# Kernel optimization log

Measured on AMD Instinct MI355X. Metric: run time of the kernel, lower is better.

## Reference

```python
import jax, jax.numpy as jnp
import numpy as np

B, S = 1, 2048
HID, INTER = 4096, 11008
HEADS, HD = 32, 128
GS = 128
EPS = 1e-6
BASE = 10000.0
IMIN, IMAX = -(2**31), 2**31 - 1


def _rope_tables():
    inv_freq = 1.0 / (BASE ** (np.arange(0, HD, 2, dtype=np.float32) / HD))
    t = np.arange(S, dtype=np.float32)
    freqs = np.outer(t, inv_freq)            # [S, HD/2]
    emb = np.concatenate([freqs, freqs], -1)  # [S, HD]
    return jnp.asarray(np.sin(emb), jnp.float32), jnp.asarray(np.cos(emb), jnp.float32)


def setup_inputs() -> dict:
    key = jax.random.key(0)
    ks = iter(jax.random.split(key, 40))
    def qset(in_f, out_f):
        qw = jax.random.randint(next(ks), (in_f // 8, out_f), IMIN, IMAX, dtype=jnp.int32)
        qz = jax.random.randint(next(ks), (in_f // GS, out_f // 8), IMIN, IMAX, dtype=jnp.int32)
        sc = jax.random.uniform(next(ks), (in_f // GS, out_f), dtype=jnp.float32) * 0.01 + 1e-3
        return qw, qz, sc
    dims = {"q": (HID, HID), "k": (HID, HID), "v": (HID, HID), "o": (HID, HID),
            "gate": (HID, INTER), "up": (HID, INTER), "down": (INTER, HID)}
    inp = {}
    for name, (i, o) in dims.items():
        qw, qz, sc = qset(i, o)
        inp["qw_" + name] = qw
        inp["qz_" + name] = qz
        inp["sc_" + name] = sc
    inp["hidden_states"] = jax.random.normal(next(ks), (B, S, HID), dtype=jnp.float32)
    inp["ln1_w"] = jnp.ones((HID,), jnp.float32)
    inp["ln2_w"] = jnp.ones((HID,), jnp.float32)
    sin, cos = _rope_tables()
    inp["sin"] = sin
    inp["cos"] = cos
    # causal additive mask, as stored in ExLlamaBuffer.attn_mask (past_len = 0)
    mask = jnp.where(jnp.tril(jnp.ones((S, S), bool)), 0.0, -1e9).astype(jnp.float32)
    inp["attn_mask"] = mask[None, None]
    return inp


def _dequant(qw, qz, sc):
    # GPTQ int4: qweight [in/8, out] packs 8 rows per int32; qzeros [groups, out/8]
    in_f, out_f = qw.shape[0] * 8, qw.shape[1]
    groups = sc.shape[0]
    sh = jnp.arange(8, dtype=jnp.int32) * 4
    w = ((qw[:, None, :] >> sh[None, :, None]) & 15)
    w = w.reshape(groups, in_f // groups, out_f).astype(jnp.float32)
    z = ((qz[:, :, None] >> sh[None, None, :]) & 15).reshape(groups, out_f).astype(jnp.float32)
    return ((w - (z + 1.0)[:, None, :]) * sc[:, None, :]).reshape(in_f, out_f)


def _rms(x, w):
    v = jnp.mean(x * x, axis=-1, keepdims=True)
    return x * jax.lax.rsqrt(v + EPS) * w


def _rot_half(x):
    x1, x2 = jnp.split(x, 2, axis=-1)
    return jnp.concatenate([-x2, x1], axis=-1)


def reference(qw_q, qz_q, sc_q, qw_k, qz_k, sc_k, qw_v, qz_v, sc_v,
              qw_o, qz_o, sc_o, qw_gate, qz_gate, sc_gate,
              qw_up, qz_up, sc_up, qw_down, qz_down, sc_down,
              hidden_states, ln1_w, ln2_w, sin, cos, attn_mask):
    lin = lambda x, a, b, c: x @ _dequant(a, b, c)
    h = hidden_states
    # attention block
    x = _rms(h, ln1_w)
    q = lin(x, qw_q, qz_q, sc_q).reshape(B, S, HEADS, HD).transpose(0, 2, 1, 3)
    k = lin(x, qw_k, qz_k, sc_k).reshape(B, S, HEADS, HD).transpose(0, 2, 1, 3)
    v = lin(x, qw_v, qz_v, sc_v).reshape(B, S, HEADS, HD).transpose(0, 2, 1, 3)
    c, s = cos[None, None], sin[None, None]  # [1,1,S,HD]
    q = q * c + _rot_half(q) * s
    k = k * c + _rot_half(k) * s
    scores = jnp.einsum('bhqd,bhkd->bhqk', q, k) / np.float32(np.sqrt(HD)) + attn_mask
    p = jax.nn.softmax(scores, axis=-1)
    o = jnp.einsum('bhqk,bhkd->bhqd', p, v).transpose(0, 2, 1, 3).reshape(B, S, HID)
    h = h + lin(o, qw_o, qz_o, sc_o)
    # MLP block
    x = _rms(h, ln2_w)
    y = jax.nn.silu(lin(x, qw_gate, qz_gate, sc_gate)) * lin(x, qw_up, qz_up, sc_up)
    return h + lin(y, qw_down, qz_down, sc_down)
```

## Files before the change

### kernel.cpp

```cpp
#include <hip/hip_runtime.h>
#include <cstdint>
#include <cstddef>

#define S_LEN 2048
#define HID   4096
#define INTER 11008
#define NHEADS 32
#define HD    128

typedef __attribute__((ext_vector_type(4))) float  f32x4;
typedef __attribute__((ext_vector_type(8))) __bf16 bf16x8;
typedef __attribute__((ext_vector_type(8))) short  s16x8;
typedef __attribute__((ext_vector_type(4))) short  s16x4;

__device__ __forceinline__ float bf2f(short s) {
  unsigned u = ((unsigned)(unsigned short)s) << 16;
  return __builtin_bit_cast(float, u);
}
__device__ __forceinline__ short f2bf(float f) {
  unsigned u = __builtin_bit_cast(unsigned, f);
  u += 0x7FFFu + ((u >> 16) & 1u);
  return (short)(u >> 16);
}
__device__ __forceinline__ f32x4 mfma16(s16x8 a, s16x8 b, f32x4 c) {
  return __builtin_amdgcn_mfma_f32_16x16x32_bf16(
      __builtin_bit_cast(bf16x8, a), __builtin_bit_cast(bf16x8, b), c, 0, 0, 0);
}
__device__ __forceinline__ void gload_lds16(const void* g, void* l) {
  __builtin_amdgcn_global_load_lds(
      (const __attribute__((address_space(1))) void*)g,
      (__attribute__((address_space(3))) void*)l, 16, 0, 0);
}

__global__ __launch_bounds__(256) void rmsnorm_kernel(const float* __restrict__ x,
                                                      const float* __restrict__ w,
                                                      short* __restrict__ out) {
  int row = blockIdx.x;
  const float* xr = x + (size_t)row * HID;
  short* orow = out + (size_t)row * HID;
  int tid = threadIdx.x;
  f32x4 v[4];
  float ss = 0.f;
#pragma unroll
  for (int i = 0; i < 4; ++i) {
    v[i] = ((const f32x4*)xr)[i * 256 + tid];
    ss += v[i][0] * v[i][0] + v[i][1] * v[i][1] + v[i][2] * v[i][2] + v[i][3] * v[i][3];
  }
#pragma unroll
  for (int off = 32; off > 0; off >>= 1) ss += __shfl_xor(ss, off);
  __shared__ float psum[4];
  if ((tid & 63) == 0) psum[tid >> 6] = ss;
  __syncthreads();
  float tot = psum[0] + psum[1] + psum[2] + psum[3];
  float r = rsqrtf(tot * (1.0f / (float)HID) + 1e-6f);
#pragma unroll
  for (int i = 0; i < 4; ++i) {
    int base = (i * 256 + tid) * 4;
    s16x4 o;
#pragma unroll
    for (int j = 0; j < 4; ++j) o[j] = f2bf(v[i][j] * r * w[base + j]);
    *(s16x4*)&orow[base] = o;
  }
}

template <int OMODE>
__global__ __launch_bounds__(256) void paired_kernel(
    const short* __restrict__ A, int lda,
    const short* __restrict__ BT, int ldb,
    void* __restrict__ Cv, int ldc,
    const float* __restrict__ base, int Kext,
    int gnx, int gny,
    const int* __restrict__ qw, const int* __restrict__ qz,
    const float* __restrict__ sc, short* __restrict__ wt,
    int N, int noff, int dnx, int dqld) {
  __shared__ short sm[4 * 4096];
  int bid = blockIdx.x;
  int gtot = gnx * gny;
  int tid = threadIdx.x;
  if (bid < gtot) {
    int cpx = gtot >> 3;
    int swz = (bid & 7) * cpx + (bid >> 3);
    int bn = swz % gnx, bm = swz / gnx;
    int lane = tid & 63, wv = tid >> 6;
    int wr = wv >> 1, wc = wv & 1;
    f32x4 acc[4][4] = {};
    int nk = Kext >> 5;
    int lr = lane >> 2, lc = lane & 3;
    const short* Abase = A + (size_t)(bm * 128) * lda;
    const short* Bbase = BT + (size_t)(bn * 128) * ldb;
    short* As0 = sm;
    short* Bs0 = sm + 8192;

    auto stage = [&](int buf, int t) {
      int k0 = t << 5;
#pragma unroll
      for (int i = 0; i < 2; ++i) {
        int r = i * 64 + wv * 16 + lr;
        gload_lds16(Abase + (size_t)r * lda + k0 + lc * 8, As0 + buf * 4096 + i * 2048 + wv * 512);
        gload_lds16(Bbase + (size_t)r * ldb + k0 + lc * 8, Bs0 + buf * 4096 + i * 2048 + wv * 512);
      }
    };
    auto compute = [&](int buf) {
      int kc = (lane >> 4) * 8;
      int ra = wr * 64 + (lane & 15);
      int rb = wc * 64 + (lane & 15);
      s16x8 af[4], bfr[4];
#pragma unroll
      for (int m = 0; m < 4; ++m) af[m] = *(const s16x8*)&As0[buf * 4096 + (ra + m * 16) * 32 + kc];
#pragma unroll
      for (int n = 0; n < 4; ++n) bfr[n] = *(const s16x8*)&Bs0[buf * 4096 + (rb + n * 16) * 32 + kc];
#pragma unroll
      for (int m = 0; m < 4; ++m)
#pragma unroll
        for (int n = 0; n < 4; ++n) acc[m][n] = mfma16(af[m], bfr[n], acc[m][n]);
    };

    stage(0, 0);
    __syncthreads();
    for (int t = 0; t < nk; ++t) {
      if (t + 1 < nk) stage((t + 1) & 1, t + 1);
      compute(t & 1);
      __syncthreads();
    }

    int row0 = bm * 128 + wr * 64 + ((lane >> 4) << 2);
    int col0 = bn * 128 + wc * 64 + (lane & 15);
#pragma unroll
    for (int m = 0; m < 4; ++m)
#pragma unroll
      for (int n = 0; n < 4; ++n)
#pragma unroll
        for (int j = 0; j < 4; ++j) {
          size_t idx = (size_t)(row0 + m * 16 + j) * ldc + col0 + n * 16;
          if (OMODE == 0)      ((short*)Cv)[idx] = f2bf(acc[m][n][j]);
          else if (OMODE == 1) ((float*)Cv)[idx] = base[idx] + acc[m][n][j];
          else if (OMODE == 2) ((float*)Cv)[idx] = ((float*)Cv)[idx] + acc[m][n][j];
          else {
            short* C = (short*)Cv;
            float g = bf2f(C[idx]);
            float sl = g / (1.f + __expf(-g));
            C[idx] = f2bf(sl * acc[m][n][j]);
          }
        }
  } else {
    int id = bid - gtot;
    int n0 = (id % dnx) * 64;
    int k0 = (id / dnx) * 64;
    int g = k0 >> 7;
    int qr0 = k0 >> 3;
#pragma unroll
    for (int i = 0; i < 2; ++i) {
      int idx = tid + i * 256;
      int r = idx >> 6;
      int n = idx & 63;
      int gc = noff + n0 + n;
      unsigned q = (unsigned)qw[(size_t)(qr0 + r) * N + gc];
      float s = sc[(size_t)g * N + gc];
      unsigned zq = (unsigned)qz[(size_t)g * (N >> 3) + (gc >> 3)];
      float zs = ((float)((zq >> ((gc & 7) * 4)) & 15u) + 1.0f) * s;
      s16x8 o;
#pragma unroll
      for (int j = 0; j < 8; ++j)
        o[j] = f2bf(fmaf((float)((q >> (4 * j)) & 15u), s, -zs));
      *(s16x8*)&sm[n * 72 + r * 8] = o;
    }
    __syncthreads();
    int n = tid >> 2;
#pragma unroll
    for (int i = 0; i < 2; ++i) {
      int c = (tid & 3) + i * 4;
      *(s16x8*)&wt[(size_t)(n0 + n) * dqld + k0 + c * 8] = *(const s16x8*)&sm[n * 72 + c * 8];
    }
  }
}

__global__ __launch_bounds__(128) void rope_kernel(short* __restrict__ q, short* __restrict__ k,
                                                   const float* __restrict__ sp,
                                                   const float* __restrict__ cp) {
  int s = blockIdx.x, h = blockIdx.y;
  short* p = (blockIdx.z ? k : q) + (size_t)s * HID + h * HD;
  int d = threadIdx.x;
  float x = bf2f(p[d]);
  float xp = bf2f(p[d ^ 64]);
  float rot = (d < 64) ? -xp : xp;
  float y = x * cp[s * HD + d] + rot * sp[s * HD + d];
  __syncthreads();
  p[d] = f2bf(y);
}

__global__ __launch_bounds__(256, 2) void attn_kernel(const short* __restrict__ qb,
                                                      const short* __restrict__ kb,
                                                      const short* __restrict__ vb,
                                                      short* __restrict__ ob) {
  int qt = (int)(gridDim.x - 1) - blockIdx.x;
  int h = blockIdx.y;
  int tid = threadIdx.x, lane = tid & 63, wv = tid >> 6;
  __shared__ short Kl[64 * 128];
  __shared__ short Vl[128 * 72];
  __shared__ short Pl[4][32 * 72];
  int q0 = qt * 128 + wv * 32;
  s16x8 qf[2][4];
#pragma unroll
  for (int m = 0; m < 2; ++m)
#pragma unroll
    for (int kf = 0; kf < 4; ++kf) {
      int r = q0 + m * 16 + (lane & 15);
      int d = kf * 32 + (lane >> 4) * 8;
      qf[m][kf] = *(const s16x8*)&qb[(size_t)r * HID + h * HD + d];
    }
  f32x4 o[2][8] = {};
  float mrow[2][4], lrow[2][4];
#pragma unroll
  for (int m = 0; m < 2; ++m)
#pragma unroll
    for (int j = 0; j < 4; ++j) { mrow[m][j] = -1e30f; lrow[m][j] = 0.f; }

  auto load_tile = [&](int kv0, s16x8* kr, s16x8* vr) {
#pragma unroll
    for (int i = 0; i < 4; ++i) {
      int cid = tid + i * 256;
      int kv = cid >> 4, c = cid & 15;
      kr[i] = *(const s16x8*)(kb + (size_t)(kv0 + kv) * HID + h * HD + c * 8);
      vr[i] = *(const s16x8*)(vb + (size_t)(kv0 + kv) * HID + h * HD + c * 8);
    }
  };
  auto store_tile = [&](const s16x8* kr, const s16x8* vr) {
#pragma unroll
    for (int i = 0; i < 4; ++i) {
      int cid = tid + i * 256;
      int kv = cid >> 4, c = cid & 15;
      *(s16x8*)((char*)Kl + kv * 256 + ((c ^ (kv & 7)) * 16)) = kr[i];
      int kvs = kv ^ ((c & 7) << 3);
#pragma unroll
      for (int j = 0; j < 8; ++j) Vl[(c * 8 + j) * 72 + kvs] = vr[i][j];
    }
  };

  const float scale = 0.08838834764831845f;
  int kv_end = qt * 128 + 128;
  s16x8 kra[4], vra[4], krb[4], vrb[4];
  load_tile(0, kra, vra);
  store_tile(kra, vra);
  __syncthreads();
  for (int kv0 = 0; kv0 < kv_end; kv0 += 64) {
    bool more = kv0 + 64 < kv_end;
    if (more) load_tile(kv0 + 64, krb, vrb);

    f32x4 sfr[2][4] = {};
    __builtin_amdgcn_s_setprio(1);
#pragma unroll
    for (int nf = 0; nf < 4; ++nf) {
      s16x8 kfr[4];
      int kvr = nf * 16 + (lane & 15);
#pragma unroll
      for (int kf = 0; kf < 4; ++kf) {
        int cc = (kf * 4 + (lane >> 4)) ^ (kvr & 7);
        kfr[kf] = *(const s16x8*)((const char*)Kl + kvr * 256 + cc * 16);
      }
#pragma unroll
      for (int m = 0; m < 2; ++m)
#pragma unroll
        for (int kf = 0; kf < 4; ++kf) sfr[m][nf] = mfma16(qf[m][kf], kfr[kf], sfr[m][nf]);
    }
    __builtin_amdgcn_s_setprio(0);
#pragma unroll
    for (int m = 0; m < 2; ++m)
#pragma unroll
      for (int j = 0; j < 4; ++j) {
        int qrow = q0 + m * 16 + (lane >> 4) * 4 + j;
        float pm = -1e30f;
#pragma unroll
        for (int nf = 0; nf < 4; ++nf) {
          int kvc = kv0 + nf * 16 + (lane & 15);
          float v = sfr[m][nf][j] * scale;
          v = (kvc <= qrow) ? v : -1e30f;
          sfr[m][nf][j] = v;
          pm = fmaxf(pm, v);
        }
#pragma unroll
        for (int off = 1; off < 16; off <<= 1) pm = fmaxf(pm, __shfl_xor(pm, off));
        float mnew = fmaxf(mrow[m][j], pm);
        float alpha = __expf(mrow[m][j] - mnew);
        mrow[m][j] = mnew;
        float rs = 0.f;
#pragma unroll
        for (int nf = 0; nf < 4; ++nf) {
          float pv = __expf(sfr[m][nf][j] - mnew);
          sfr[m][nf][j] = pv;
          rs += pv;
        }
#pragma unroll
        for (int off = 1; off < 16; off <<= 1) rs += __shfl_xor(rs, off);
        lrow[m][j] = lrow[m][j] * alpha + rs;
#pragma unroll
        for (int nd = 0; nd < 8; ++nd) o[m][nd][j] *= alpha;
      }
#pragma unroll
    for (int m = 0; m < 2; ++m)
#pragma unroll
      for (int nf = 0; nf < 4; ++nf)
#pragma unroll
        for (int j = 0; j < 4; ++j)
          Pl[wv][(m * 16 + (lane >> 4) * 4 + j) * 72 + nf * 16 + (lane & 15)] =
              f2bf(sfr[m][nf][j]);
    s16x8 pa[2][2];
#pragma unroll
    for (int m = 0; m < 2; ++m)
#pragma unroll
      for (int kf = 0; kf < 2; ++kf)
        pa[m][kf] = *(const s16x8*)&Pl[wv][(m * 16 + (lane & 15)) * 72 + kf * 32 + (lane >> 4) * 8];
    __builtin_amdgcn_s_setprio(1);
#pragma unroll
    for (int nd = 0; nd < 8; ++nd) {
      s16x8 vf[2];
      int drow = nd * 16 + (lane & 15);
      int key = ((drow >> 3) & 7) << 3;
#pragma unroll
      for (int kf = 0; kf < 2; ++kf)
        vf[kf] = *(const s16x8*)&Vl[drow * 72 + ((kf * 32 + (lane >> 4) * 8) ^ key)];
#pragma unroll
      for (int m = 0; m < 2; ++m)
#pragma unroll
        for (int kf = 0; kf < 2; ++kf) o[m][nd] = mfma16(pa[m][kf], vf[kf], o[m][nd]);
    }
    __builtin_amdgcn_s_setprio(0);
    __syncthreads();
    if (more) store_tile(krb, vrb);
    __syncthreads();
  }
#pragma unroll
  for (int m = 0; m < 2; ++m)
#pragma unroll
    for (int nd = 0; nd < 8; ++nd)
#pragma unroll
      for (int j = 0; j < 4; ++j) {
        int r = q0 + m * 16 + (lane >> 4) * 4 + j;
        int c = h * HD + nd * 16 + (lane & 15);
        ob[(size_t)r * HID + c] = f2bf(o[m][nd][j] / lrow[m][j]);
      }
}

extern "C" void kernel_launch(void* const* d_in, const int* in_sizes, int n_in,
                              void* d_out, int out_size, void* d_ws, size_t ws_size,
                              hipStream_t stream) {
  const int* qw[7]; const int* qz[7]; const float* sc[7];
  for (int i = 0; i < 7; ++i) {
    qw[i] = (const int*)d_in[i * 3 + 0];
    qz[i] = (const int*)d_in[i * 3 + 1];
    sc[i] = (const float*)d_in[i * 3 + 2];
  }
  const float* hin  = (const float*)d_in[21];
  const float* ln1  = (const float*)d_in[22];
  const float* ln2  = (const float*)d_in[23];
  const float* sinp = (const float*)d_in[24];
  const float* cosp = (const float*)d_in[25];
  float* out = (float*)d_out;

  char* ws = (char*)d_ws;
  const size_t MB = 1024 * 1024;
  short* XB    = (short*)(ws);
  short* WA    = (short*)(ws + 16 * MB);
  short* WB    = (short*)(ws + 48 * MB);
  short* KB    = (short*)(ws + 80 * MB);
  short* VB    = (short*)(ws + 96 * MB);
  short* OB    = (short*)(ws + 112 * MB);
  short* GATEB = (short*)(ws + 80 * MB);
  short* UPB   = XB;
  (void)UPB;
  short* QBd   = (short*)d_out;

  dim3 blk(256);
  const int noffs[3] = {0, 4096, 8192};
  const int nexts[3] = {4096, 4096, 2816};

  rmsnorm_kernel<<<S_LEN, blk, 0, stream>>>(hin, ln1, XB);
  paired_kernel<0><<<4096, blk, 0, stream>>>(nullptr, 0, nullptr, 0, nullptr, 0, nullptr, 0,
                                             0, 0, qw[0], qz[0], sc[0], WA, HID, 0, 64, HID);
  paired_kernel<0><<<512 + 4096, blk, 0, stream>>>(XB, HID, WA, HID, QBd, HID, nullptr, HID,
                                                   32, 16, qw[1], qz[1], sc[1], WB, HID, 0, 64, HID);
  paired_kernel<0><<<512 + 4096, blk, 0, stream>>>(XB, HID, WB, HID, KB, HID, nullptr, HID,
                                                   32, 16, qw[2], qz[2], sc[2], WA, HID, 0, 64, HID);
  paired_kernel<0><<<512 + 4096, blk, 0, stream>>>(XB, HID, WA, HID, VB, HID, nullptr, HID,
                                                   32, 16, qw[3], qz[3], sc[3], WB, HID, 0, 64, HID);
  rope_kernel<<<dim3(S_LEN, NHEADS, 2), dim3(128), 0, stream>>>(QBd, KB, sinp, cosp);
  attn_kernel<<<dim3(S_LEN / 128, NHEADS), blk, 0, stream>>>(QBd, KB, VB, OB);
  paired_kernel<1><<<512 + 4096, blk, 0, stream>>>(OB, HID, WB, HID, out, HID, hin, HID,
                                                   32, 16, qw[4], qz[4], sc[4], WA, INTER, 0, 64, HID);
  rmsnorm_kernel<<<S_LEN, blk, 0, stream>>>(out, ln2, XB);

  paired_kernel<0><<<512 + 4096, blk, 0, stream>>>(XB, HID, WA, HID, GATEB + 0, INTER, nullptr, HID,
                                                   32, 16, qw[5], qz[5], sc[5], WB, INTER, 0, 64, HID);
  paired_kernel<3><<<512 + 4096, blk, 0, stream>>>(XB, HID, WB, HID, GATEB + 0, INTER, nullptr, HID,
                                                   32, 16, qw[4], qz[4], sc[4], WA, INTER, 4096, 64, HID);
  paired_kernel<0><<<512 + 4096, blk, 0, stream>>>(XB, HID, WA, HID, GATEB + 4096, INTER, nullptr, HID,
                                                   32, 16, qw[5], qz[5], sc[5], WB, INTER, 4096, 64, HID);
  paired_kernel<3><<<512 + 2816, blk, 0, stream>>>(XB, HID, WB, HID, GATEB + 4096, INTER, nullptr, HID,
                                                   32, 16, qw[4], qz[4], sc[4], WA, INTER, 8192, 44, HID);
  paired_kernel<0><<<352 + 2816, blk, 0, stream>>>(XB, HID, WA, HID, GATEB + 8192, INTER, nullptr, HID,
                                                   22, 16, qw[5], qz[5], sc[5], WB, INTER, 8192, 44, HID);
  paired_kernel<3><<<352 + 4096, blk, 0, stream>>>(XB, HID, WB, HID, GATEB + 8192, INTER, nullptr, HID,
                                                   22, 16, qw[6], qz[6], sc[6], WA, HID, 0, 64, 4096);
  paired_kernel<2><<<512 + 4096, blk, 0, stream>>>(GATEB + 0, INTER, WA, 4096, out, HID, nullptr, 4096,
                                                   32, 16,
                                                   qw[6] + (size_t)(4096 >> 3) * HID,
                                                   qz[6] + (size_t)(4096 >> 7) * (HID / 8),
                                                   sc[6] + (size_t)(4096 >> 7) * HID,
                                                   WB, HID, 0, 64, 4096);
  paired_kernel<2><<<512 + 2816, blk, 0, stream>>>(GATEB + 4096, INTER, WB, 4096, out, HID, nullptr, 4096,
                                                   32, 16,
                                                   qw[6] + (size_t)(8192 >> 3) * HID,
                                                   qz[6] + (size_t)(8192 >> 7) * (HID / 8),
                                                   sc[6] + (size_t)(8192 >> 7) * HID,
                                                   WA, HID, 0, 64, 2816);
  paired_kernel<2><<<512, blk, 0, stream>>>(GATEB + 8192, INTER, WA, 2816, out, HID, nullptr, 2816,
                                            32, 16, nullptr, nullptr, nullptr, nullptr, HID, 0, 1, HID);
}
```

Baseline: 1.386 ms.

## Fuse int4 dequantization into GEMM B-tile staging instead of separate dequant pass

```diff
diff --git a/kernel.cpp b/kernel.cpp
--- a/kernel.cpp
+++ b/kernel.cpp
@@ -64,97 +64,46 @@
 }
 
 template <int OMODE>
-__global__ __launch_bounds__(256) void paired_kernel(
+__global__ __launch_bounds__(256) void dqgemm_kernel(
     const short* __restrict__ A, int lda,
-    const short* __restrict__ BT, int ldb,
+    const int* __restrict__ qw, const int* __restrict__ qz,
+    const float* __restrict__ sc, int N,
     void* __restrict__ Cv, int ldc,
-    const float* __restrict__ base, int Kext,
-    int gnx, int gny,
-    const int* __restrict__ qw, const int* __restrict__ qz,
-    const float* __restrict__ sc, short* __restrict__ wt,
-    int N, int noff, int dnx, int dqld) {
-  __shared__ short sm[4 * 4096];
+    const float* __restrict__ base, int Kext, int gnx) {
+  __shared__ short As[2][128 * 32];
+  __shared__ short Bs[2][4 * 128 * 8];
+  int tid = threadIdx.x;
+  int lane = tid & 63, wv = tid >> 6;
+  int wr = wv >> 1, wc = wv & 1;
+  int gtot = gnx * 16;
   int bid = blockIdx.x;
-  int gtot = gnx * gny;
-  int tid = threadIdx.x;
-  if (bid < gtot) {
-    int cpx = gtot >> 3;
-    int swz = (bid & 7) * cpx + (bid >> 3);
-    int bn = swz % gnx, bm = swz / gnx;
-    int lane = tid & 63, wv = tid >> 6;
-    int wr = wv >> 1, wc = wv & 1;
-    f32x4 acc[4][4] = {};
-    int nk = Kext >> 5;
-    int lr = lane >> 2, lc = lane & 3;
-    const short* Abase = A + (size_t)(bm * 128) * lda;
-    const short* Bbase = BT + (size_t)(bn * 128) * ldb;
-    short* As0 = sm;
-    short* Bs0 = sm + 8192;
-
-    auto stage = [&](int buf, int t) {
-      int k0 = t << 5;
-#pragma unroll
-      for (int i = 0; i < 2; ++i) {
-        int r = i * 64 + wv * 16 + lr;
-        gload_lds16(Abase + (size_t)r * lda + k0 + lc * 8, As0 + buf * 4096 + i * 2048 + wv * 512);
-        gload_lds16(Bbase + (size_t)r * ldb + k0 + lc * 8, Bs0 + buf * 4096 + i * 2048 + wv * 512);
-      }
-    };
-    auto compute = [&](int buf) {
-      int kc = (lane >> 4) * 8;
-      int ra = wr * 64 + (lane & 15);
-      int rb = wc * 64 + (lane & 15);
-      s16x8 af[4], bfr[4];
-#pragma unroll
-      for (int m = 0; m < 4; ++m) af[m] = *(const s16x8*)&As0[buf * 4096 + (ra + m * 16) * 32 + kc];
-#pragma unroll
-      for (int n = 0; n < 4; ++n) bfr[n] = *(const s16x8*)&Bs0[buf * 4096 + (rb + n * 16) * 32 + kc];
-#pragma unroll
-      for (int m = 0; m < 4; ++m)
-#pragma unroll
-        for (int n = 0; n < 4; ++n) acc[m][n] = mfma16(af[m], bfr[n], acc[m][n]);
-    };
-
-    stage(0, 0);
-    __syncthreads();
-    for (int t = 0; t < nk; ++t) {
-      if (t + 1 < nk) stage((t + 1) & 1, t + 1);
-      compute(t & 1);
-      __syncthreads();
-    }
-
-    int row0 = bm * 128 + wr * 64 + ((lane >> 4) << 2);
-    int col0 = bn * 128 + wc * 64 + (lane & 15);
-#pragma unroll
-    for (int m = 0; m < 4; ++m)
-#pragma unroll
-      for (int n = 0; n < 4; ++n)
-#pragma unroll
-        for (int j = 0; j < 4; ++j) {
-          size_t idx = (size_t)(row0 + m * 16 + j) * ldc + col0 + n * 16;
-          if (OMODE == 0)      ((short*)Cv)[idx] = f2bf(acc[m][n][j]);
-          else if (OMODE == 1) ((float*)Cv)[idx] = base[idx] + acc[m][n][j];
-          else if (OMODE == 2) ((float*)Cv)[idx] = ((float*)Cv)[idx] + acc[m][n][j];
-          else {
-            short* C = (short*)Cv;
-            float g = bf2f(C[idx]);
-            float sl = g / (1.f + __expf(-g));
-            C[idx] = f2bf(sl * acc[m][n][j]);
-          }
-        }
-  } else {
-    int id = bid - gtot;
-    int n0 = (id % dnx) * 64;
-    int k0 = (id / dnx) * 64;
+  int swz = (bid & 7) * (gtot >> 3) + (bid >> 3);
+  int bn = swz % gnx, bm = swz / gnx;
+  f32x4 acc[4][4] = {};
+  int nk = Kext >> 5;
+  int lr = lane >> 2, lc = lane & 3;
+  const short* Abase = A + (size_t)(bm * 128) * lda;
+  int ncol0 = bn * 128;
+
+  auto stageA = [&](int buf, int t) {
+    int k0 = t << 5;
+#pragma unroll
+    for (int i = 0; i < 2; ++i) {
+      int r = i * 64 + wv * 16 + lr;
+      gload_lds16(Abase + (size_t)r * lda + k0 + lc * 8, &As[buf][i * 2048 + wv * 512]);
+    }
+  };
+  auto stageB = [&](int buf, int t) {
+    int k0 = t << 5;
+    int qrow0 = k0 >> 3;
     int g = k0 >> 7;
-    int qr0 = k0 >> 3;
 #pragma unroll
     for (int i = 0; i < 2; ++i) {
       int idx = tid + i * 256;
-      int r = idx >> 6;
-      int n = idx & 63;
-      int gc = noff + n0 + n;
-      unsigned q = (unsigned)qw[(size_t)(qr0 + r) * N + gc];
+      int r = idx >> 7;
+      int col = idx & 127;
+      int gc = ncol0 + col;
+      unsigned q = (unsigned)qw[(size_t)(qrow0 + r) * N + gc];
       float s = sc[(size_t)g * N + gc];
       unsigned zq = (unsigned)qz[(size_t)g * (N >> 3) + (gc >> 3)];
       float zs = ((float)((zq >> ((gc & 7) * 4)) & 15u) + 1.0f) * s;
@@ -162,16 +111,52 @@
 #pragma unroll
       for (int j = 0; j < 8; ++j)
         o[j] = f2bf(fmaf((float)((q >> (4 * j)) & 15u), s, -zs));
-      *(s16x8*)&sm[n * 72 + r * 8] = o;
-    }
+      *(s16x8*)&Bs[buf][(r * 128 + col) * 8] = o;
+    }
+  };
+  auto compute = [&](int buf) {
+    int kc = lane >> 4;
+    int ra = wr * 64 + (lane & 15);
+    s16x8 af[4], bfr[4];
+#pragma unroll
+    for (int m = 0; m < 4; ++m)
+      af[m] = *(const s16x8*)&As[buf][(ra + m * 16) * 32 + kc * 8];
+#pragma unroll
+    for (int n = 0; n < 4; ++n)
+      bfr[n] = *(const s16x8*)&Bs[buf][(kc * 128 + wc * 64 + n * 16 + (lane & 15)) * 8];
+#pragma unroll
+    for (int m = 0; m < 4; ++m)
+#pragma unroll
+      for (int n = 0; n < 4; ++n) acc[m][n] = mfma16(af[m], bfr[n], acc[m][n]);
+  };
+
+  stageA(0, 0); stageB(0, 0);
+  __syncthreads();
+  for (int t = 0; t < nk; ++t) {
+    if (t + 1 < nk) { stageA((t + 1) & 1, t + 1); stageB((t + 1) & 1, t + 1); }
+    compute(t & 1);
     __syncthreads();
-    int n = tid >> 2;
-#pragma unroll
-    for (int i = 0; i < 2; ++i) {
-      int c = (tid & 3) + i * 4;
-      *(s16x8*)&wt[(size_t)(n0 + n) * dqld + k0 + c * 8] = *(const s16x8*)&sm[n * 72 + c * 8];
-    }
-  }
+  }
+
+  int row0 = bm * 128 + wr * 64 + ((lane >> 4) << 2);
+  int col0 = ncol0 + wc * 64 + (lane & 15);
+#pragma unroll
+  for (int m = 0; m < 4; ++m)
+#pragma unroll
+    for (int n = 0; n < 4; ++n)
+#pragma unroll
+      for (int j = 0; j < 4; ++j) {
+        size_t idx = (size_t)(row0 + m * 16 + j) * ldc + col0 + n * 16;
+        float a = acc[m][n][j];
+        if (OMODE == 0)      ((short*)Cv)[idx] = f2bf(a);
+        else if (OMODE == 1) ((float*)Cv)[idx] = base[idx] + a;
+        else if (OMODE == 2) ((float*)Cv)[idx] = ((float*)Cv)[idx] + a;
+        else {
+          short* C = (short*)Cv;
+          float g = bf2f(C[idx]);
+          C[idx] = f2bf(g / (1.f + __expf(-g)) * a);
+        }
+      }
 }
 
 __global__ __launch_bounds__(128) void rope_kernel(short* __restrict__ q, short* __restrict__ k,
@@ -358,60 +343,24 @@
 
   char* ws = (char*)d_ws;
   const size_t MB = 1024 * 1024;
-  short* XB    = (short*)(ws);
-  short* WA    = (short*)(ws + 16 * MB);
-  short* WB    = (short*)(ws + 48 * MB);
-  short* KB    = (short*)(ws + 80 * MB);
-  short* VB    = (short*)(ws + 96 * MB);
-  short* OB    = (short*)(ws + 112 * MB);
-  short* GATEB = (short*)(ws + 80 * MB);
-  short* UPB   = XB;
-  (void)UPB;
-  short* QBd   = (short*)d_out;
+  short* XB = (short*)(ws);
+  short* QB = (short*)(ws + 16 * MB);
+  short* KB = (short*)(ws + 32 * MB);
+  short* VB = (short*)(ws + 48 * MB);
+  short* OB = (short*)(ws + 64 * MB);
+  short* YB = (short*)(ws + 80 * MB);
 
   dim3 blk(256);
-  const int noffs[3] = {0, 4096, 8192};
-  const int nexts[3] = {4096, 4096, 2816};
 
   rmsnorm_kernel<<<S_LEN, blk, 0, stream>>>(hin, ln1, XB);
-  paired_kernel<0><<<4096, blk, 0, stream>>>(nullptr, 0, nullptr, 0, nullptr, 0, nullptr, 0,
-                                             0, 0, qw[0], qz[0], sc[0], WA, HID, 0, 64, HID);
-  paired_kernel<0><<<512 + 4096, blk, 0, stream>>>(XB, HID, WA, HID, QBd, HID, nullptr, HID,
-                                                   32, 16, qw[1], qz[1], sc[1], WB, HID, 0, 64, HID);
-  paired_kernel<0><<<512 + 4096, blk, 0, stream>>>(XB, HID, WB, HID, KB, HID, nullptr, HID,
-                                                   32, 16, qw[2], qz[2], sc[2], WA, HID, 0, 64, HID);
-  paired_kernel<0><<<512 + 4096, blk, 0, stream>>>(XB, HID, WA, HID, VB, HID, nullptr, HID,
-                                                   32, 16, qw[3], qz[3], sc[3], WB, HID, 0, 64, HID);
-  rope_kernel<<<dim3(S_LEN, NHEADS, 2), dim3(128), 0, stream>>>(QBd, KB, sinp, cosp);
-  attn_kernel<<<dim3(S_LEN / 128, NHEADS), blk, 0, stream>>>(QBd, KB, VB, OB);
-  paired_kernel<1><<<512 + 4096, blk, 0, stream>>>(OB, HID, WB, HID, out, HID, hin, HID,
-                                                   32, 16, qw[4], qz[4], sc[4], WA, INTER, 0, 64, HID);
+  dqgemm_kernel<0><<<512, blk, 0, stream>>>(XB, HID, qw[0], qz[0], sc[0], HID, QB, HID, nullptr, HID, 32);
+  dqgemm_kernel<0><<<512, blk, 0, stream>>>(XB, HID, qw[1], qz[1], sc[1], HID, KB, HID, nullptr, HID, 32);
+  dqgemm_kernel<0><<<512, blk, 0, stream>>>(XB, HID, qw[2], qz[2], sc[2], HID, VB, HID, nullptr, HID, 32);
+  rope_kernel<<<dim3(S_LEN, NHEADS, 2), dim3(128), 0, stream>>>(QB, KB, sinp, cosp);
+  attn_kernel<<<dim3(S_LEN / 128, NHEADS), blk, 0, stream>>>(QB, KB, VB, OB);
+  dqgemm_kernel<1><<<512, blk, 0, stream>>>(OB, HID, qw[3], qz[3], sc[3], HID, out, HID, hin, HID, 32);
   rmsnorm_kernel<<<S_LEN, blk, 0, stream>>>(out, ln2, XB);
-
-  paired_kernel<0><<<512 + 4096, blk, 0, stream>>>(XB, HID, WA, HID, GATEB + 0, INTER, nullptr, HID,
-                                                   32, 16, qw[5], qz[5], sc[5], WB, INTER, 0, 64, HID);
-  paired_kernel<3><<<512 + 4096, blk, 0, stream>>>(XB, HID, WB, HID, GATEB + 0, INTER, nullptr, HID,
-                                                   32, 16, qw[4], qz[4], sc[4], WA, INTER, 4096, 64, HID);
-  paired_kernel<0><<<512 + 4096, blk, 0, stream>>>(XB, HID, WA, HID, GATEB + 4096, INTER, nullptr, HID,
-                                                   32, 16, qw[5], qz[5], sc[5], WB, INTER, 4096, 64, HID);
-  paired_kernel<3><<<512 + 2816, blk, 0, stream>>>(XB, HID, WB, HID, GATEB + 4096, INTER, nullptr, HID,
-                                                   32, 16, qw[4], qz[4], sc[4], WA, INTER, 8192, 44, HID);
-  paired_kernel<0><<<352 + 2816, blk, 0, stream>>>(XB, HID, WA, HID, GATEB + 8192, INTER, nullptr, HID,
-                                                   22, 16, qw[5], qz[5], sc[5], WB, INTER, 8192, 44, HID);
-  paired_kernel<3><<<352 + 4096, blk, 0, stream>>>(XB, HID, WB, HID, GATEB + 8192, INTER, nullptr, HID,
-                                                   22, 16, qw[6], qz[6], sc[6], WA, HID, 0, 64, 4096);
-  paired_kernel<2><<<512 + 4096, blk, 0, stream>>>(GATEB + 0, INTER, WA, 4096, out, HID, nullptr, 4096,
-                                                   32, 16,
-                                                   qw[6] + (size_t)(4096 >> 3) * HID,
-                                                   qz[6] + (size_t)(4096 >> 7) * (HID / 8),
-                                                   sc[6] + (size_t)(4096 >> 7) * HID,
-                                                   WB, HID, 0, 64, 4096);
-  paired_kernel<2><<<512 + 2816, blk, 0, stream>>>(GATEB + 4096, INTER, WB, 4096, out, HID, nullptr, 4096,
-                                                   32, 16,
-                                                   qw[6] + (size_t)(8192 >> 3) * HID,
-                                                   qz[6] + (size_t)(8192 >> 7) * (HID / 8),
-                                                   sc[6] + (size_t)(8192 >> 7) * HID,
-                                                   WA, HID, 0, 64, 2816);
-  paired_kernel<2><<<512, blk, 0, stream>>>(GATEB + 8192, INTER, WA, 2816, out, HID, nullptr, 2816,
-                                            32, 16, nullptr, nullptr, nullptr, nullptr, HID, 0, 1, HID);
-}
+  dqgemm_kernel<0><<<1376, blk, 0, stream>>>(XB, HID, qw[4], qz[4], sc[4], INTER, YB, INTER, nullptr, HID, 86);
+  dqgemm_kernel<3><<<1376, blk, 0, stream>>>(XB, HID, qw[5], qz[5], sc[5], INTER, YB, INTER, nullptr, HID, 86);
+  dqgemm_kernel<2><<<512, blk, 0, stream>>>(YB, INTER, qw[6], qz[6], sc[6], HID, out, HID, nullptr, INTER, 32);
+}
```

After: 1.642 ms. +18.5%, slower.

## Switch intermediates and MFMA from bf16 to fp16 with magic-number dequant

Applied to the files above, without the earlier changes.

```diff
diff --git a/kernel.cpp b/kernel.cpp
--- a/kernel.cpp
+++ b/kernel.cpp
@@ -8,23 +8,22 @@
 #define NHEADS 32
 #define HD    128
 
-typedef __attribute__((ext_vector_type(4))) float  f32x4;
-typedef __attribute__((ext_vector_type(8))) __bf16 bf16x8;
-typedef __attribute__((ext_vector_type(8))) short  s16x8;
-typedef __attribute__((ext_vector_type(4))) short  s16x4;
-
-__device__ __forceinline__ float bf2f(short s) {
-  unsigned u = ((unsigned)(unsigned short)s) << 16;
-  return __builtin_bit_cast(float, u);
-}
-__device__ __forceinline__ short f2bf(float f) {
-  unsigned u = __builtin_bit_cast(unsigned, f);
-  u += 0x7FFFu + ((u >> 16) & 1u);
-  return (short)(u >> 16);
-}
-__device__ __forceinline__ f32x4 mfma16(s16x8 a, s16x8 b, f32x4 c) {
-  return __builtin_amdgcn_mfma_f32_16x16x32_bf16(
-      __builtin_bit_cast(bf16x8, a), __builtin_bit_cast(bf16x8, b), c, 0, 0, 0);
+typedef __attribute__((ext_vector_type(4))) float    f32x4;
+typedef __attribute__((ext_vector_type(8))) _Float16 f16x8;
+typedef __attribute__((ext_vector_type(2))) _Float16 h2;
+typedef __attribute__((ext_vector_type(8))) short    s16x8;
+typedef __attribute__((ext_vector_type(4))) short    s16x4;
+typedef __attribute__((ext_vector_type(4))) unsigned u32x4;
+
+__device__ __forceinline__ float h2f(short s) {
+  return (float)__builtin_bit_cast(_Float16, s);
+}
+__device__ __forceinline__ short f2h(float f) {
+  return __builtin_bit_cast(short, (_Float16)f);
+}
+__device__ __forceinline__ f32x4 mfma16f(s16x8 a, s16x8 b, f32x4 c) {
+  return __builtin_amdgcn_mfma_f32_16x16x32_f16(
+      __builtin_bit_cast(f16x8, a), __builtin_bit_cast(f16x8, b), c, 0, 0, 0);
 }
 __device__ __forceinline__ void gload_lds16(const void* g, void* l) {
   __builtin_amdgcn_global_load_lds(
@@ -58,7 +57,7 @@
     int base = (i * 256 + tid) * 4;
     s16x4 o;
 #pragma unroll
-    for (int j = 0; j < 4; ++j) o[j] = f2bf(v[i][j] * r * w[base + j]);
+    for (int j = 0; j < 4; ++j) o[j] = f2h(v[i][j] * r * w[base + j]);
     *(s16x4*)&orow[base] = o;
   }
 }
@@ -112,7 +111,7 @@
 #pragma unroll
       for (int m = 0; m < 4; ++m)
 #pragma unroll
-        for (int n = 0; n < 4; ++n) acc[m][n] = mfma16(af[m], bfr[n], acc[m][n]);
+        for (int n = 0; n < 4; ++n) acc[m][n] = mfma16f(af[m], bfr[n], acc[m][n]);
     };
 
     stage(0, 0);
@@ -132,14 +131,14 @@
 #pragma unroll
         for (int j = 0; j < 4; ++j) {
           size_t idx = (size_t)(row0 + m * 16 + j) * ldc + col0 + n * 16;
-          if (OMODE == 0)      ((short*)Cv)[idx] = f2bf(acc[m][n][j]);
+          if (OMODE == 0)      ((short*)Cv)[idx] = f2h(acc[m][n][j]);
           else if (OMODE == 1) ((float*)Cv)[idx] = base[idx] + acc[m][n][j];
           else if (OMODE == 2) ((float*)Cv)[idx] = ((float*)Cv)[idx] + acc[m][n][j];
           else {
             short* C = (short*)Cv;
-            float g = bf2f(C[idx]);
+            float g = h2f(C[idx]);
             float sl = g / (1.f + __expf(-g));
-            C[idx] = f2bf(sl * acc[m][n][j]);
+            C[idx] = f2h(sl * acc[m][n][j]);
           }
         }
   } else {
@@ -157,12 +156,20 @@
       unsigned q = (unsigned)qw[(size_t)(qr0 + r) * N + gc];
       float s = sc[(size_t)g * N + gc];
       unsigned zq = (unsigned)qz[(size_t)g * (N >> 3) + (gc >> 3)];
-      float zs = ((float)((zq >> ((gc & 7) * 4)) & 15u) + 1.0f) * s;
-      s16x8 o;
-#pragma unroll
-      for (int j = 0; j < 8; ++j)
-        o[j] = f2bf(fmaf((float)((q >> (4 * j)) & 15u), s, -zs));
-      *(s16x8*)&sm[n * 72 + r * 8] = o;
+      int z = (int)((zq >> ((gc & 7) * 4)) & 15u);
+      _Float16 hz = (_Float16)(float)(1025 + z);
+      _Float16 hs = (_Float16)s;
+      h2 zc = {hz, hz}, s2 = {hs, hs};
+      u32x4 ov;
+#pragma unroll
+      for (int j = 0; j < 4; ++j) {
+        unsigned u = q >> (8 * j);
+        unsigned pb = (u & 0xFu) | ((u & 0xF0u) << 12) | 0x64006400u;
+        h2 w = __builtin_bit_cast(h2, pb);
+        h2 rr = (w - zc) * s2;
+        ov[j] = __builtin_bit_cast(unsigned, rr);
+      }
+      *(u32x4*)&sm[n * 72 + r * 8] = ov;
     }
     __syncthreads();
     int n = tid >> 2;
@@ -180,12 +187,12 @@
   int s = blockIdx.x, h = blockIdx.y;
   short* p = (blockIdx.z ? k : q) + (size_t)s * HID + h * HD;
   int d = threadIdx.x;
-  float x = bf2f(p[d]);
-  float xp = bf2f(p[d ^ 64]);
+  float x = h2f(p[d]);
+  float xp = h2f(p[d ^ 64]);
   float rot = (d < 64) ? -xp : xp;
   float y = x * cp[s * HD + d] + rot * sp[s * HD + d];
   __syncthreads();
-  p[d] = f2bf(y);
+  p[d] = f2h(y);
 }
 
 __global__ __launch_bounds__(256, 2) void attn_kernel(const short* __restrict__ qb,
@@ -260,7 +267,7 @@
 #pragma unroll
       for (int m = 0; m < 2; ++m)
 #pragma unroll
-        for (int kf = 0; kf < 4; ++kf) sfr[m][nf] = mfma16(qf[m][kf], kfr[kf], sfr[m][nf]);
+        for (int kf = 0; kf < 4; ++kf) sfr[m][nf] = mfma16f(qf[m][kf], kfr[kf], sfr[m][nf]);
     }
     __builtin_amdgcn_s_setprio(0);
 #pragma unroll
@@ -302,7 +309,7 @@
 #pragma unroll
         for (int j = 0; j < 4; ++j)
           Pl[wv][(m * 16 + (lane >> 4) * 4 + j) * 72 + nf * 16 + (lane & 15)] =
-              f2bf(sfr[m][nf][j]);
+              f2h(sfr[m][nf][j]);
     s16x8 pa[2][2];
 #pragma unroll
     for (int m = 0; m < 2; ++m)
@@ -321,7 +328,7 @@
 #pragma unroll
       for (int m = 0; m < 2; ++m)
 #pragma unroll
-        for (int kf = 0; kf < 2; ++kf) o[m][nd] = mfma16(pa[m][kf], vf[kf], o[m][nd]);
+        for (int kf = 0; kf < 2; ++kf) o[m][nd] = mfma16f(pa[m][kf], vf[kf], o[m][nd]);
     }
     __builtin_amdgcn_s_setprio(0);
     __syncthreads();
@@ -336,7 +343,7 @@
       for (int j = 0; j < 4; ++j) {
         int r = q0 + m * 16 + (lane >> 4) * 4 + j;
         int c = h * HD + nd * 16 + (lane & 15);
-        ob[(size_t)r * HID + c] = f2bf(o[m][nd][j] / lrow[m][j]);
+        ob[(size_t)r * HID + c] = f2h(o[m][nd][j] / lrow[m][j]);
       }
 }
 
@@ -365,13 +372,9 @@
   short* VB    = (short*)(ws + 96 * MB);
   short* OB    = (short*)(ws + 112 * MB);
   short* GATEB = (short*)(ws + 80 * MB);
-  short* UPB   = XB;
-  (void)UPB;
   short* QBd   = (short*)d_out;
 
   dim3 blk(256);
-  const int noffs[3] = {0, 4096, 8192};
-  const int nexts[3] = {4096, 4096, 2816};
 
   rmsnorm_kernel<<<S_LEN, blk, 0, stream>>>(hin, ln1, XB);
   paired_kernel<0><<<4096, blk, 0, stream>>>(nullptr, 0, nullptr, 0, nullptr, 0, nullptr, 0,
```

Measured after the change: 1.416 ms. +2.1%, slower.
